# Optimization experiments

Hardware: AMD Instinct MI355X
Metric: run time of the kernel (lower is better)

Reference implementation:

```python
import jax, jax.numpy as jnp
import numpy as np
from jax import lax

# Model dims (match init_kwargs / Mamba2 defaults)
B = 8; C_IN = 512; C_OUT = 512; H = 32; W = 32; L = H * W
D_STATE = 64; D_CONV = 4; EXPAND = 2; HEADDIM = 64
D_INNER = EXPAND * C_IN            # 1024
NHEADS = D_INNER // HEADDIM        # 16
D_XBC = D_INNER + 2 * D_STATE      # 1152 (ngroups=1)
D_IN_PROJ = 2 * D_INNER + 2 * D_STATE + NHEADS
EPS = 1e-5


def setup_inputs() -> dict:
    key = jax.random.key(0)
    ks = jax.random.split(key, 16)
    x = jax.random.normal(ks[0], (B, C_IN, H, W), jnp.float32)
    ln_w = jnp.ones((C_IN,), jnp.float32)
    ln_b = jnp.zeros((C_IN,), jnp.float32)
    in_proj_w = jax.random.normal(ks[1], (D_IN_PROJ, C_IN), jnp.float32) * 0.02
    conv1d_w = jax.random.normal(ks[2], (D_XBC, D_CONV), jnp.float32) * 0.2
    conv1d_b = jax.random.normal(ks[3], (D_XBC,), jnp.float32) * 0.02
    dt0 = jax.random.uniform(ks[4], (NHEADS,), jnp.float32, 1e-3, 0.1)
    dt_bias = jnp.log(jnp.expm1(dt0))  # inverse softplus init
    A_log = jnp.log(jax.random.uniform(ks[5], (NHEADS,), jnp.float32, 1.0, 16.0))
    D = jax.random.normal(ks[6], (NHEADS,), jnp.float32)
    rms_w = jnp.ones((D_INNER,), jnp.float32)
    out_proj_w = jax.random.normal(ks[7], (C_IN, D_INNER), jnp.float32) * 0.02
    conv2d_w = jax.random.normal(ks[8], (C_OUT, C_IN), jnp.float32) * 0.04
    conv2d_b = jnp.zeros((C_OUT,), jnp.float32)
    bn_g = jnp.ones((C_OUT,), jnp.float32)
    bn_b = jnp.zeros((C_OUT,), jnp.float32)
    bn_mean = jnp.zeros((C_OUT,), jnp.float32)
    bn_var = jnp.ones((C_OUT,), jnp.float32)
    return dict(x=x, ln_w=ln_w, ln_b=ln_b, in_proj_w=in_proj_w, conv1d_w=conv1d_w,
                conv1d_b=conv1d_b, dt_bias=dt_bias, A_log=A_log, D=D, rms_w=rms_w,
                out_proj_w=out_proj_w, conv2d_w=conv2d_w, conv2d_b=conv2d_b,
                bn_g=bn_g, bn_b=bn_b, bn_mean=bn_mean, bn_var=bn_var)


def reference(x, ln_w, ln_b, in_proj_w, conv1d_w, conv1d_b, dt_bias, A_log, D,
              rms_w, out_proj_w, conv2d_w, conv2d_b, bn_g, bn_b, bn_mean, bn_var):
    Bb, C, Hh, Ww = x.shape
    Ltok = Hh * Ww
    # tokens: (B, L, C)
    t = x.reshape(Bb, C, Ltok).transpose(0, 2, 1)
    # LayerNorm over channel dim
    mu = jnp.mean(t, -1, keepdims=True)
    var = jnp.mean(jnp.square(t - mu), -1, keepdims=True)
    xn = (t - mu) * lax.rsqrt(var + EPS) * ln_w + ln_b
    # Mamba2 in_proj -> [z, xBC, dt]
    zxbcdt = jnp.einsum('blc,dc->bld', xn, in_proj_w)
    z = zxbcdt[..., :D_INNER]
    xBC = zxbcdt[..., D_INNER:D_INNER + D_XBC]
    dt = zxbcdt[..., D_INNER + D_XBC:]                       # (B, L, nheads)
    # causal depthwise conv1d + silu
    conv = lax.conv_general_dilated(xBC.transpose(0, 2, 1), conv1d_w[:, None, :],
                                    window_strides=(1,), padding=[(D_CONV - 1, 0)],
                                    feature_group_count=D_XBC)
    xBC = jax.nn.silu(conv.transpose(0, 2, 1) + conv1d_b)
    xh = xBC[..., :D_INNER].reshape(Bb, Ltok, NHEADS, HEADDIM)
    Bm = xBC[..., D_INNER:D_INNER + D_STATE]                 # (B, L, d_state)
    Cm = xBC[..., D_INNER + D_STATE:]
    dt = jax.nn.softplus(dt + dt_bias)
    A = -jnp.exp(A_log)                                      # (nheads,)
    # selective scan (SSD recurrence), state h: (B, nheads, headdim, d_state)
    def step(h, inp):
        xt, dtt, Bt, Ct = inp
        dA = jnp.exp(dtt * A)                                # (B, nheads)
        h = h * dA[..., None, None] + jnp.einsum('bh,bhp,bs->bhps', dtt, xt, Bt)
        y = jnp.einsum('bhps,bs->bhp', h, Ct)
        return h, y
    h0 = jnp.zeros((Bb, NHEADS, HEADDIM, D_STATE), x.dtype)
    xs = (xh.transpose(1, 0, 2, 3), dt.transpose(1, 0, 2),
          Bm.transpose(1, 0, 2), Cm.transpose(1, 0, 2))
    _, ys = lax.scan(step, h0, xs)
    y = ys.transpose(1, 0, 2, 3) + D[None, None, :, None] * xh
    y = y.reshape(Bb, Ltok, D_INNER)
    # gated RMSNorm
    y = y * jax.nn.silu(z)
    y = y * lax.rsqrt(jnp.mean(y * y, -1, keepdims=True) + EPS) * rms_w
    out = jnp.einsum('bld,cd->blc', y, out_proj_w)
    img = out.transpose(0, 2, 1).reshape(Bb, C, Hh, Ww)
    # 1x1 conv + BN (inference) + ReLU
    c = jnp.einsum('bchw,oc->bohw', img, conv2d_w) + conv2d_b[None, :, None, None]
    c = (c - bn_mean[None, :, None, None]) * lax.rsqrt(bn_var + EPS)[None, :, None, None]
    c = c * bn_g[None, :, None, None] + bn_b[None, :, None, None]
    return jax.nn.relu(c)
```

## Files before the change

kernel.cpp:

```cpp
#include <hip/hip_runtime.h>
#include <hip/hip_bf16.h>

#define NB 8
#define LL 1024
#define CIN 512
#define DIN 1024
#define DXBC 1152
#define DPROJ 2192
#define NPADW 2304
#define NUSE 2176
#define NHH 16
#define HDD 64
#define DST 64
#define NCHUNK 16
#define QCH 64
#define XBCS 1024
#define CTT 8
#define DTB 16

typedef unsigned short u16;
typedef unsigned int u32;
typedef __bf16 bf16x8 __attribute__((ext_vector_type(8)));
typedef float f32x4 __attribute__((ext_vector_type(4)));
typedef u16 u16x8 __attribute__((ext_vector_type(8)));

__device__ __forceinline__ float bf2f(u16 u) {
    u32 x = ((u32)u) << 16; float f; __builtin_memcpy(&f, &x, 4); return f;
}
__device__ __forceinline__ u16 f2bf(float f) {
    u32 x; __builtin_memcpy(&x, &f, 4);
    u32 r = x + 0x7fff + ((x >> 16) & 1);
    return (u16)(r >> 16);
}

__device__ __forceinline__ void gload16(const u16* g, u16* l) {
    __builtin_amdgcn_global_load_lds((__attribute__((address_space(1))) void*)(g),
                                     (__attribute__((address_space(3))) void*)(l), 16, 0, 0);
}

__device__ __forceinline__ int swz(int row, int cb) {
    return row * 64 + ((cb ^ ((row & 7) << 4)) >> 1);
}

#define PREP_WIN_BLKS 4608
#define PREP_WC2_BLKS 1024
__global__ __launch_bounds__(256) void prep_all(const float* __restrict__ ipw, u16* __restrict__ Win,
                                                const float* __restrict__ c2w, u16* __restrict__ Wc2,
                                                const float* __restrict__ cb, const float* __restrict__ g,
                                                const float* __restrict__ bb, const float* __restrict__ mean,
                                                const float* __restrict__ var,
                                                float* __restrict__ scale, float* __restrict__ shift) {
    int bid = blockIdx.x;
    if (bid < PREP_WIN_BLKS) {
        int i = bid * 256 + threadIdx.x;
        Win[i] = (i < DPROJ * CIN) ? f2bf(ipw[i]) : (u16)0;
    } else if (bid < PREP_WIN_BLKS + PREP_WC2_BLKS) {
        int i = (bid - PREP_WIN_BLKS) * 256 + threadIdx.x;
        Wc2[i] = f2bf(c2w[i]);
    } else {
        int i = (bid - PREP_WIN_BLKS - PREP_WC2_BLKS) * 256 + threadIdx.x;
        if (i < CIN) {
            float rs = rsqrtf(var[i] + 1e-5f);
            float sc = g[i] * rs;
            scale[i] = sc;
            shift[i] = (cb[i] - mean[i]) * sc + bb[i];
        }
    }
}

__global__ __launch_bounds__(256) void woutT_conv(const float* __restrict__ s,
                                                  const float* __restrict__ rw,
                                                  u16* __restrict__ dt) {
    __shared__ float tile[64][65];
    int bc = blockIdx.x & 7, bd = blockIdx.x >> 3;
    int c0 = bc * 64, d0 = bd * 64;
    int t = threadIdx.x;
    int r4 = t >> 6, cc = t & 63;
#pragma unroll
    for (int rr = 0; rr < 16; ++rr) {
        int row = r4 * 16 + rr;
        tile[row][cc] = s[(size_t)(c0 + row) * DIN + d0 + cc];
    }
    __syncthreads();
#pragma unroll
    for (int rr = 0; rr < 16; ++rr) {
        int row = r4 * 16 + rr;
        dt[(size_t)(d0 + row) * CIN + c0 + cc] = f2bf(tile[cc][row] * rw[d0 + row]);
    }
}

__global__ __launch_bounds__(256) void ln_kernel(const float* __restrict__ x,
                                                 const float* __restrict__ lw,
                                                 const float* __restrict__ lb,
                                                 u16* __restrict__ xn) {
    __shared__ u16 tile[CIN * 33];
    __shared__ float psum[8][32], psq[8][32], muA[32], rsA[32];
    int bid = blockIdx.x;
    int b = bid >> 5, hw0 = (bid & 31) * 32;
    int t = threadIdx.x;
    int hw = t & 31, cg = t >> 5;
    const float* xb = x + (size_t)b * CIN * LL + hw0 + hw;
    float s = 0.f, sq = 0.f;
    for (int r = 0; r < CIN / 8; ++r) {
        int c = r * 8 + cg;
        float v = xb[(size_t)c * LL];
        s += v; sq += v * v;
        tile[c * 33 + hw] = f2bf(v);
    }
    psum[cg][hw] = s; psq[cg][hw] = sq;
    __syncthreads();
    if (t < 32) {
        float ss = 0.f, qq = 0.f;
        for (int g = 0; g < 8; ++g) { ss += psum[g][t]; qq += psq[g][t]; }
        float mu = ss * (1.f / CIN);
        float var = qq * (1.f / CIN) - mu * mu;
        muA[t] = mu; rsA[t] = rsqrtf(var + 1e-5f);
    }
    __syncthreads();
    for (int r = 0; r < 64; ++r) {
        int idx = r * 256 + t;
        int c = idx & (CIN - 1);
        int hh = idx >> 9;
        float v = (bf2f(tile[c * 33 + hh]) - muA[hh]) * rsA[hh] * lw[c] + lb[c];
        xn[((size_t)(b * LL + hw0 + hh)) * CIN + c] = f2bf(v);
    }
}

template <int EPI>
__global__ __launch_bounds__(256) void gemm_bt(const u16* __restrict__ A, const u16* __restrict__ Bw,
                                               void* __restrict__ Cout, int M, int N, int K, int ldc,
                                               int nx,
                                               const float* __restrict__ scale,
                                               const float* __restrict__ shift,
                                               const float* __restrict__ PS) {
    __shared__ u16 As[2][128 * 64], Bs[2][64 * 64];
    __shared__ float rsl[64];
    int t = threadIdx.x;
    int lane = t & 63, wave = t >> 6;
    int nblk = gridDim.x;
    int qq = nblk >> 3, rm = nblk & 7;
    int xcd = blockIdx.x & 7, idx = blockIdx.x >> 3;
    int swzb = (xcd < rm ? xcd * (qq + 1) : rm * (qq + 1) + (xcd - rm) * qq) + idx;
    int m0 = (swzb / nx) * 128, n0 = (swzb % nx) * 64;
    int wr = wave >> 1, wc = wave & 1;
    f32x4 acc[4][2];
    for (int m = 0; m < 4; ++m)
        for (int n = 0; n < 2; ++n)
            for (int q = 0; q < 4; ++q) acc[m][n][q] = 0.f;

    if (EPI == 1) {
        if (t < 64) {
            int tok = n0 + t;
            int b = tok >> 10, rem = tok & 1023;
            int c = rem >> 6, ii = rem & 63;
            float s = 0.f;
#pragma unroll
            for (int h = 0; h < NHH; ++h)
                s += PS[(size_t)(((b << 4) + h) * 16 + c) * 64 + ii];
            rsl[t] = rsqrtf(s * (1.f / DIN) + 1e-5f);
        }
        __syncthreads();
    }

    const u16* Arow = A + (size_t)m0 * K;
    const u16* Brow = Bw + (size_t)n0 * K;
    int s4 = lane >> 4;
    int rr = lane & 15;

    auto STAGE = [&](int buf, int k0) {
#pragma unroll
        for (int j = 0; j < 4; ++j) {
            int e = j * 256 + t;
            int r = e >> 3, sr = e & 7;
            int src = (sr ^ (r & 7)) * 8;
            gload16(Arow + (size_t)r * K + k0 + src, &As[buf][e * 8]);
        }
#pragma unroll
        for (int j = 0; j < 2; ++j) {
            int e = j * 256 + t;
            int r = e >> 3, sr = e & 7;
            int src = (sr ^ (r & 7)) * 8;
            gload16(Brow + (size_t)r * K + k0 + src, &Bs[buf][e * 8]);
        }
    };

    STAGE(0, 0);
    int NK = K >> 6, cur = 0;
    for (int kt = 0; kt < NK; ++kt) {
        if (kt + 1 < NK) {
            STAGE(cur ^ 1, (kt + 1) << 6);
            asm volatile("s_waitcnt vmcnt(6)" ::: "memory");
        } else {
            asm volatile("s_waitcnt vmcnt(0)" ::: "memory");
        }
        __builtin_amdgcn_s_barrier();
        __builtin_amdgcn_sched_barrier(0);
#pragma unroll
        for (int kk = 0; kk < 2; ++kk) {
            bf16x8 af[4], bfr[2];
#pragma unroll
            for (int m = 0; m < 4; ++m) {
                int row = wr * 64 + m * 16 + rr;
                int ss = (kk * 4 + s4) ^ (row & 7);
                af[m] = *(const bf16x8*)&As[cur][row * 64 + ss * 8];
            }
#pragma unroll
            for (int n = 0; n < 2; ++n) {
                int row = wc * 32 + n * 16 + rr;
                int ss = (kk * 4 + s4) ^ (row & 7);
                bfr[n] = *(const bf16x8*)&Bs[cur][row * 64 + ss * 8];
            }
#pragma unroll
            for (int m = 0; m < 4; ++m)
#pragma unroll
                for (int n = 0; n < 2; ++n)
                    acc[m][n] = __builtin_amdgcn_mfma_f32_16x16x32_bf16(af[m], bfr[n], acc[m][n], 0, 0, 0);
        }
        __builtin_amdgcn_s_barrier();
        cur ^= 1;
    }
    int fq = lane >> 4, fr = lane & 15;
#pragma unroll
    for (int m = 0; m < 4; ++m) {
#pragma unroll
        for (int n = 0; n < 2; ++n) {
            int col = n0 + wc * 32 + n * 16 + fr;
#pragma unroll
            for (int q = 0; q < 4; ++q) {
                int row = m0 + wr * 64 + m * 16 + fq * 4 + q;
                float v = acc[m][n][q];
                if (EPI == 0) {
                    ((u16*)Cout)[(size_t)row * ldc + col] = f2bf(v);
                } else {
                    v = v * rsl[col - n0];
                    v = v * scale[row] + shift[row];
                    v = v > 0.f ? v : 0.f;
                    ((float*)Cout)[((size_t)(col >> 10)) * (CIN * LL) + (size_t)row * LL + (col & 1023)] = v;
                }
            }
        }
    }
}

__global__ __launch_bounds__(288) void convdt(const u16* __restrict__ zx,
                                              const float* __restrict__ w,
                                              const float* __restrict__ bias,
                                              u16* __restrict__ xbc,
                                              u16* __restrict__ Bc, u16* __restrict__ Cc,
                                              const u16* __restrict__ xn,
                                              const float* __restrict__ wproj,
                                              const float* __restrict__ dt_bias,
                                              const float* __restrict__ A_log,
                                              float2* __restrict__ dtda) {
    int bid = blockIdx.x;
    int t = threadIdx.x;
    if (bid < NB * (LL / CTT)) {
        int b = bid >> 7;
        int l0 = (bid & 127) * CTT;
        bool isX = t < 256;
        int ch = isX ? t * 4 : 1024 + (t - 256) * 4;

        float4 wv0 = *(const float4*)&w[(ch + 0) * 4];
        float4 wv1 = *(const float4*)&w[(ch + 1) * 4];
        float4 wv2 = *(const float4*)&w[(ch + 2) * 4];
        float4 wv3 = *(const float4*)&w[(ch + 3) * 4];
        float4 bv = *(const float4*)&bias[ch];

        ushort4 xin[CTT + 3];
        const u16* src = zx + (size_t)(b * LL + l0 - 3) * NPADW + DIN + ch;
#pragma unroll
        for (int i = 0; i < CTT + 3; ++i) {
            ushort4 v = {0, 0, 0, 0};
            if (l0 + i - 3 >= 0) v = *(const ushort4*)(src + (size_t)i * NPADW);
            xin[i] = v;
        }
#pragma unroll
        for (int i = 0; i < CTT; ++i) {
            int tok = b * LL + l0 + i;
            float a0 = bv.x + bf2f(xin[i].x) * wv0.x + bf2f(xin[i + 1].x) * wv0.y +
                       bf2f(xin[i + 2].x) * wv0.z + bf2f(xin[i + 3].x) * wv0.w;
            float a1 = bv.y + bf2f(xin[i].y) * wv1.x + bf2f(xin[i + 1].y) * wv1.y +
                       bf2f(xin[i + 2].y) * wv1.z + bf2f(xin[i + 3].y) * wv1.w;
            float a2 = bv.z + bf2f(xin[i].z) * wv2.x + bf2f(xin[i + 1].z) * wv2.y +
                       bf2f(xin[i + 2].z) * wv2.z + bf2f(xin[i + 3].z) * wv2.w;
            float a3 = bv.w + bf2f(xin[i].w) * wv3.x + bf2f(xin[i + 1].w) * wv3.y +
                       bf2f(xin[i + 2].w) * wv3.z + bf2f(xin[i + 3].w) * wv3.w;
            float s0 = a0 / (1.f + __expf(-a0));
            float s1 = a1 / (1.f + __expf(-a1));
            float s2 = a2 / (1.f + __expf(-a2));
            float s3 = a3 / (1.f + __expf(-a3));
            ushort4 o;
            o.x = f2bf(s0); o.y = f2bf(s1); o.z = f2bf(s2); o.w = f2bf(s3);
            if (isX) {
                *(ushort4*)&xbc[(size_t)tok * XBCS + ch] = o;
            } else {
                int s = ch - 1024;
                if (s < DST) *(ushort4*)&Bc[(size_t)tok * DST + s] = o;
                else         *(ushort4*)&Cc[(size_t)tok * DST + (s - DST)] = o;
            }
        }
    } else {
        if (t >= 256) return;
        int h = t >> 4, part = t & 15;
        int tok0 = (bid - NB * (LL / CTT)) * DTB;
        const float* wr = wproj + (size_t)(DIN + DXBC + h) * CIN + part * 32;
        float4 wv[8];
#pragma unroll
        for (int i = 0; i < 8; ++i) wv[i] = *(const float4*)&wr[i * 4];
        const float* wf = (const float*)wv;
        float dtb = dt_bias[h];
        float An = -__expf(A_log[h]);
#pragma unroll
        for (int tl = 0; tl < DTB; ++tl) {
            int tok = tok0 + tl;
            const u16* xr = xn + (size_t)tok * CIN + part * 32;
            u16x8 xv0 = *(const u16x8*)&xr[0];
            u16x8 xv1 = *(const u16x8*)&xr[8];
            u16x8 xv2 = *(const u16x8*)&xr[16];
            u16x8 xv3 = *(const u16x8*)&xr[24];
            float s = 0.f;
#pragma unroll
            for (int i = 0; i < 8; ++i) s += bf2f(xv0[i]) * wf[i];
#pragma unroll
            for (int i = 0; i < 8; ++i) s += bf2f(xv1[i]) * wf[8 + i];
#pragma unroll
            for (int i = 0; i < 8; ++i) s += bf2f(xv2[i]) * wf[16 + i];
#pragma unroll
            for (int i = 0; i < 8; ++i) s += bf2f(xv3[i]) * wf[24 + i];
            s += __shfl_xor(s, 1, 64);
            s += __shfl_xor(s, 2, 64);
            s += __shfl_xor(s, 4, 64);
            s += __shfl_xor(s, 8, 64);
            if (part == 0) {
                float si = s + dtb;
                float dtv = si > 15.f ? si : __logf(1.f + __expf(si));
                float2 dd; dd.x = dtv; dd.y = dtv * An;
                dtda[(size_t)tok * NHH + h] = dd;
            }
        }
    }
}

__global__ __launch_bounds__(256) void ssd_chunk(const u16* __restrict__ Bcb,
                                                 const u16* __restrict__ Ccb,
                                                 const u16* __restrict__ xbc,
                                                 const float2* __restrict__ dtda,
                                                 u16* __restrict__ yi,
                                                 u16* __restrict__ DHb,
                                                 float* __restrict__ ESA,
                                                 float* __restrict__ DC) {
    __shared__ u16 Bt[4096], Ct[4096], XT[4096], BTt[4096], Gt[4096];
    __shared__ float Sar[64], dtvA[64], wA[64];
    int tau = blockIdx.x;
    int b = tau >> 8, h = (tau >> 4) & 15, c = tau & 15;
    int t0g = b * LL + c * QCH;
    int t = threadIdx.x, lane = t & 63, wave = t >> 6;
    int row = t >> 2, q = t & 3;

    {
        const u16* bp = Bcb + (size_t)(t0g + row) * DST + q * 16;
        const u16* cp = Ccb + (size_t)(t0g + row) * DST + q * 16;
        u16x8 b0v = *(const u16x8*)bp;
        u16x8 b1v = *(const u16x8*)(bp + 8);
        *(u16x8*)&Bt[swz(row, q * 32)] = b0v;
        *(u16x8*)&Bt[swz(row, q * 32 + 16)] = b1v;
        u16x8 c0v = *(const u16x8*)cp;
        u16x8 c1v = *(const u16x8*)(cp + 8);
        *(u16x8*)&Ct[swz(row, q * 32)] = c0v;
        *(u16x8*)&Ct[swz(row, q * 32 + 16)] = c1v;
        const u16* xp = xbc + (size_t)(t0g + row) * XBCS + h * HDD + q * 16;
        u16x8 x0 = *(const u16x8*)xp;
        u16x8 x1 = *(const u16x8*)(xp + 8);
#pragma unroll
        for (int e = 0; e < 8; ++e) XT[swz(q * 16 + e, row * 2)] = x0[e];
#pragma unroll
        for (int e = 0; e < 8; ++e) XT[swz(q * 16 + 8 + e, row * 2)] = x1[e];
    }
    if (t < 64) {
        float2 dd = dtda[(size_t)(t0g + t) * NHH + h];
        float s = dd.y;
#pragma unroll
        for (int off = 1; off < 64; off <<= 1) {
            float u = __shfl_up(s, off, 64);
            if (t >= off) s += u;
        }
        float SQ = __shfl(s, 63, 64);
        Sar[t] = s; dtvA[t] = dd.x;
        wA[t] = __expf(SQ - s) * dd.x;
        ESA[(size_t)tau * 64 + t] = __expf(s);
        if (t == 0) DC[tau] = __expf(SQ);
    }
    __syncthreads();

    int R = wave >> 1, Cq = wave & 1, rr = lane & 15, sg = lane >> 4;
    f32x4 g[2][2];
#pragma unroll
    for (int mi = 0; mi < 2; ++mi)
#pragma unroll
        for (int ni = 0; ni < 2; ++ni)
#pragma unroll
            for (int r = 0; r < 4; ++r) g[mi][ni][r] = 0.f;
#pragma unroll
    for (int kt = 0; kt < 2; ++kt) {
        int cb = kt * 64 + sg * 16;
        bf16x8 a0 = *(const bf16x8*)&Ct[swz(R * 32 + rr, cb)];
        bf16x8 a1 = *(const bf16x8*)&Ct[swz(R * 32 + 16 + rr, cb)];
        bf16x8 b0 = *(const bf16x8*)&Bt[swz(Cq * 32 + rr, cb)];
        bf16x8 b1 = *(const bf16x8*)&Bt[swz(Cq * 32 + 16 + rr, cb)];
        g[0][0] = __builtin_amdgcn_mfma_f32_16x16x32_bf16(a0, b0, g[0][0], 0, 0, 0);
        g[0][1] = __builtin_amdgcn_mfma_f32_16x16x32_bf16(a0, b1, g[0][1], 0, 0, 0);
        g[1][0] = __builtin_amdgcn_mfma_f32_16x16x32_bf16(a1, b0, g[1][0], 0, 0, 0);
        g[1][1] = __builtin_amdgcn_mfma_f32_16x16x32_bf16(a1, b1, g[1][1], 0, 0, 0);
    }
#pragma unroll
    for (int mi = 0; mi < 2; ++mi)
#pragma unroll
        for (int ni = 0; ni < 2; ++ni)
#pragma unroll
            for (int r = 0; r < 4; ++r) {
                int i = R * 32 + mi * 16 + sg * 4 + r;
                int j = Cq * 32 + ni * 16 + rr;
                float v = (i >= j) ? g[mi][ni][r] * __expf(Sar[i] - Sar[j]) * dtvA[j] : 0.f;
                Gt[swz(i, j * 2)] = f2bf(v);
            }
#pragma unroll
    for (int half = 0; half < 2; ++half) {
        u16x8 bv = *(const u16x8*)&Bt[swz(row, q * 32 + half * 16)];
#pragma unroll
        for (int e = 0; e < 8; ++e)
            BTt[swz(q * 16 + half * 8 + e, row * 2)] = f2bf(bf2f(bv[e]) * wA[row]);
    }
    __syncthreads();

    f32x4 y[2][2], dh[2][2];
#pragma unroll
    for (int mi = 0; mi < 2; ++mi)
#pragma unroll
        for (int ni = 0; ni < 2; ++ni)
#pragma unroll
            for (int r = 0; r < 4; ++r) { y[mi][ni][r] = 0.f; dh[mi][ni][r] = 0.f; }
#pragma unroll
    for (int kt = 0; kt < 2; ++kt) {
        int cb = kt * 64 + sg * 16;
        bf16x8 xb0 = *(const bf16x8*)&XT[swz(Cq * 32 + rr, cb)];
        bf16x8 xb1 = *(const bf16x8*)&XT[swz(Cq * 32 + 16 + rr, cb)];
        bf16x8 ga0 = *(const bf16x8*)&Gt[swz(R * 32 + rr, cb)];
        bf16x8 ga1 = *(const bf16x8*)&Gt[swz(R * 32 + 16 + rr, cb)];
        bf16x8 ba0 = *(const bf16x8*)&BTt[swz(R * 32 + rr, cb)];
        bf16x8 ba1 = *(const bf16x8*)&BTt[swz(R * 32 + 16 + rr, cb)];
        y[0][0] = __builtin_amdgcn_mfma_f32_16x16x32_bf16(ga0, xb0, y[0][0], 0, 0, 0);
        y[0][1] = __builtin_amdgcn_mfma_f32_16x16x32_bf16(ga0, xb1, y[0][1], 0, 0, 0);
        y[1][0] = __builtin_amdgcn_mfma_f32_16x16x32_bf16(ga1, xb0, y[1][0], 0, 0, 0);
        y[1][1] = __builtin_amdgcn_mfma_f32_16x16x32_bf16(ga1, xb1, y[1][1], 0, 0, 0);
        dh[0][0] = __builtin_amdgcn_mfma_f32_16x16x32_bf16(ba0, xb0, dh[0][0], 0, 0, 0);
        dh[0][1] = __builtin_amdgcn_mfma_f32_16x16x32_bf16(ba0, xb1, dh[0][1], 0, 0, 0);
        dh[1][0] = __builtin_amdgcn_mfma_f32_16x16x32_bf16(ba1, xb0, dh[1][0], 0, 0, 0);
        dh[1][1] = __builtin_amdgcn_mfma_f32_16x16x32_bf16(ba1, xb1, dh[1][1], 0, 0, 0);
    }
#pragma unroll
    for (int mi = 0; mi < 2; ++mi)
#pragma unroll
        for (int ni = 0; ni < 2; ++ni)
#pragma unroll
            for (int r = 0; r < 4; ++r) {
                int i = R * 32 + mi * 16 + sg * 4 + r;
                int p = Cq * 32 + ni * 16 + rr;
                yi[(size_t)(t0g + i) * DIN + h * HDD + p] = f2bf(y[mi][ni][r]);
                DHb[(size_t)tau * 4096 + i * 64 + p] = f2bf(dh[mi][ni][r]);
            }
}

__global__ __launch_bounds__(256) void ssd_carry(const u16* __restrict__ DHb,
                                                 const float* __restrict__ DC,
                                                 u16* __restrict__ HPREV) {
    int bid = blockIdx.x;
    int bh = bid >> 1, ph = bid & 1;
    int t = threadIdx.x;
    int s = t >> 2, p0 = ph * 32 + (t & 3) * 8;
    size_t base = (size_t)bh * NCHUNK * 4096 + s * 64 + p0;
    float Hv[8] = {0.f, 0.f, 0.f, 0.f, 0.f, 0.f, 0.f, 0.f};
    for (int c = 0; c < NCHUNK; ++c) {
        size_t off = base + (size_t)c * 4096;
        u16x8 hp;
#pragma unroll
        for (int e = 0; e < 8; ++e) hp[e] = f2bf(Hv[e]);
        *(u16x8*)&HPREV[off] = hp;
        float d = DC[bh * NCHUNK + c];
        u16x8 dv = *(const u16x8*)&DHb[off];
#pragma unroll
        for (int e = 0; e < 8; ++e) Hv[e] = d * Hv[e] + bf2f(dv[e]);
    }
}

__global__ __launch_bounds__(256) void ssd_final(const u16* __restrict__ Ccb,
                                                 const float* __restrict__ ESA,
                                                 const u16* __restrict__ HPREV,
                                                 const u16* __restrict__ xbc,
                                                 const u16* __restrict__ zx,
                                                 const float* __restrict__ Dp,
                                                 u16* __restrict__ yi,
                                                 float* __restrict__ PS) {
    __shared__ u16 C2t[4096], HT[4096];
    __shared__ float smem_ps[2][64];
    int tau = blockIdx.x;
    int b = tau >> 8, h = (tau >> 4) & 15, c = tau & 15;
    int t0g = b * LL + c * QCH;
    int t = threadIdx.x, lane = t & 63, wave = t >> 6;
    int row = t >> 2, q = t & 3;
    {
        float esa = ESA[(size_t)tau * 64 + row];
        const u16* cp = Ccb + (size_t)(t0g + row) * DST + q * 16;
#pragma unroll
        for (int half = 0; half < 2; ++half) {
            u16x8 cv = *(const u16x8*)(cp + half * 8);
            u16x8 oc;
#pragma unroll
            for (int e = 0; e < 8; ++e) oc[e] = f2bf(bf2f(cv[e]) * esa);
            *(u16x8*)&C2t[swz(row, q * 32 + half * 16)] = oc;
            u16x8 hv = *(const u16x8*)&HPREV[(size_t)tau * 4096 + row * 64 + q * 16 + half * 8];
#pragma unroll
            for (int e = 0; e < 8; ++e) HT[swz(q * 16 + half * 8 + e, row * 2)] = hv[e];
        }
    }
    __syncthreads();
    int R = wave >> 1, Cq = wave & 1, rr = lane & 15, sg = lane >> 4;
    float Dh = Dp[h];
    f32x4 acc[2][2];
#pragma unroll
    for (int mi = 0; mi < 2; ++mi)
#pragma unroll
        for (int ni = 0; ni < 2; ++ni)
#pragma unroll
            for (int r = 0; r < 4; ++r) {
                int i = R * 32 + mi * 16 + sg * 4 + r;
                int p = Cq * 32 + ni * 16 + rr;
                acc[mi][ni][r] = bf2f(yi[(size_t)(t0g + i) * DIN + h * HDD + p]);
            }
#pragma unroll
    for (int kt = 0; kt < 2; ++kt) {
        int cb = kt * 64 + sg * 16;
        bf16x8 a0 = *(const bf16x8*)&C2t[swz(R * 32 + rr, cb)];
        bf16x8 a1 = *(const bf16x8*)&C2t[swz(R * 32 + 16 + rr, cb)];
        bf16x8 b0 = *(const bf16x8*)&HT[swz(Cq * 32 + rr, cb)];
        bf16x8 b1 = *(const bf16x8*)&HT[swz(Cq * 32 + 16 + rr, cb)];
        acc[0][0] = __builtin_amdgcn_mfma_f32_16x16x32_bf16(a0, b0, acc[0][0], 0, 0, 0);
        acc[0][1] = __builtin_amdgcn_mfma_f32_16x16x32_bf16(a0, b1, acc[0][1], 0, 0, 0);
        acc[1][0] = __builtin_amdgcn_mfma_f32_16x16x32_bf16(a1, b0, acc[1][0], 0, 0, 0);
        acc[1][1] = __builtin_amdgcn_mfma_f32_16x16x32_bf16(a1, b1, acc[1][1], 0, 0, 0);
    }
    float ps[2][4];
#pragma unroll
    for (int mi = 0; mi < 2; ++mi)
#pragma unroll
        for (int r = 0; r < 4; ++r) ps[mi][r] = 0.f;
#pragma unroll
    for (int mi = 0; mi < 2; ++mi)
#pragma unroll
        for (int ni = 0; ni < 2; ++ni)
#pragma unroll
            for (int r = 0; r < 4; ++r) {
                int i = R * 32 + mi * 16 + sg * 4 + r;
                int p = Cq * 32 + ni * 16 + rr;
                size_t tok = t0g + i;
                int col = h * HDD + p;
                float xf = bf2f(xbc[tok * XBCS + col]);
                float zf = bf2f(zx[tok * NPADW + col]);
                float yo = (acc[mi][ni][r] + Dh * xf) * (zf / (1.f + __expf(-zf)));
                yi[tok * DIN + col] = f2bf(yo);
                ps[mi][r] += yo * yo;
            }
#pragma unroll
    for (int mi = 0; mi < 2; ++mi)
#pragma unroll
        for (int r = 0; r < 4; ++r) {
            float s2 = ps[mi][r];
            s2 += __shfl_xor(s2, 1, 64);
            s2 += __shfl_xor(s2, 2, 64);
            s2 += __shfl_xor(s2, 4, 64);
            s2 += __shfl_xor(s2, 8, 64);
            if (rr == 0) smem_ps[Cq][R * 32 + mi * 16 + sg * 4 + r] = s2;
        }
    __syncthreads();
    if (t < 64) PS[(size_t)tau * 64 + t] = smem_ps[0][t] + smem_ps[1][t];
}

extern "C" void kernel_launch(void* const* d_in, const int* in_sizes, int n_in,
                              void* d_out, int out_size, void* d_ws, size_t ws_size,
                              hipStream_t stream) {
    const float* x         = (const float*)d_in[0];
    const float* ln_w      = (const float*)d_in[1];
    const float* ln_b      = (const float*)d_in[2];
    const float* in_proj_w = (const float*)d_in[3];
    const float* conv1d_w  = (const float*)d_in[4];
    const float* conv1d_b  = (const float*)d_in[5];
    const float* dt_bias   = (const float*)d_in[6];
    const float* A_log     = (const float*)d_in[7];
    const float* Dp        = (const float*)d_in[8];
    const float* rms_w     = (const float*)d_in[9];
    const float* out_proj_w= (const float*)d_in[10];
    const float* conv2d_w  = (const float*)d_in[11];
    const float* conv2d_b  = (const float*)d_in[12];
    const float* bn_g      = (const float*)d_in[13];
    const float* bn_b      = (const float*)d_in[14];
    const float* bn_mean   = (const float*)d_in[15];
    const float* bn_var    = (const float*)d_in[16];

    const int TOK = NB * LL;
    const int NTAU = NB * NHH * NCHUNK;
    char* ws = (char*)d_ws;
    size_t off = 0;
    auto alloc = [&](size_t bytes) {
        void* p = ws + off;
        off += (bytes + 255) & ~(size_t)255;
        return p;
    };
    u16*   Win   = (u16*)alloc((size_t)NPADW * CIN * 2);
    u16*   WoutT = (u16*)alloc((size_t)DIN * CIN * 2);
    u16*   Wc2   = (u16*)alloc((size_t)CIN * CIN * 2);
    u16*   WCMB  = (u16*)alloc((size_t)CIN * DIN * 2);
    u16*   XN    = (u16*)alloc((size_t)TOK * CIN * 2);
    u16*   ZX    = (u16*)alloc((size_t)TOK * NPADW * 2);
    u16*   XBC   = (u16*)alloc((size_t)TOK * XBCS * 2);
    u16*   Bcb   = (u16*)alloc((size_t)TOK * DST * 2);
    u16*   Ccb   = (u16*)alloc((size_t)TOK * DST * 2);
    float2* DTDA = (float2*)alloc((size_t)TOK * NHH * 8);
    u16*   YI    = (u16*)alloc((size_t)TOK * DIN * 2);
    u16*   DHb   = (u16*)alloc((size_t)NTAU * 4096 * 2);
    u16*   HPREV = (u16*)alloc((size_t)NTAU * 4096 * 2);
    float* ESA   = (float*)alloc((size_t)NTAU * 64 * 4);
    float* PS    = (float*)alloc((size_t)NTAU * 64 * 4);
    float* DC    = (float*)alloc((size_t)NTAU * 4);
    float* BNSC  = (float*)alloc(CIN * 4);
    float* BNSH  = (float*)alloc(CIN * 4);

    prep_all<<<PREP_WIN_BLKS + PREP_WC2_BLKS + 2, 256, 0, stream>>>(
        in_proj_w, Win, conv2d_w, Wc2, conv2d_b, bn_g, bn_b, bn_mean, bn_var, BNSC, BNSH);
    woutT_conv<<<128, 256, 0, stream>>>(out_proj_w, rms_w, WoutT);
    gemm_bt<0><<<(CIN / 128) * (DIN / 64), 256, 0, stream>>>(Wc2, WoutT, WCMB, CIN, DIN, CIN, DIN,
                                                             DIN / 64, nullptr, nullptr, nullptr);

    ln_kernel<<<256, 256, 0, stream>>>(x, ln_w, ln_b, XN);

    gemm_bt<0><<<(TOK / 128) * (NUSE / 64), 256, 0, stream>>>(XN, Win, ZX, TOK, NUSE, CIN, NPADW,
                                                              NUSE / 64, nullptr, nullptr, nullptr);

    convdt<<<NB * (LL / CTT) + TOK / DTB, 288, 0, stream>>>(ZX, conv1d_w, conv1d_b, XBC, Bcb, Ccb,
                                                            XN, in_proj_w, dt_bias, A_log, DTDA);

    ssd_chunk<<<NTAU, 256, 0, stream>>>(Bcb, Ccb, XBC, DTDA, YI, DHb, ESA, DC);
    ssd_carry<<<256, 256, 0, stream>>>(DHb, DC, HPREV);
    ssd_final<<<NTAU, 256, 0, stream>>>(Ccb, ESA, HPREV, XBC, ZX, Dp, YI, PS);

    gemm_bt<1><<<(CIN / 128) * (TOK / 64), 256, 0, stream>>>(WCMB, YI, d_out, CIN, TOK, DIN, 0,
                                                             TOK / 64, BNSC, BNSH, PS);
}
```

Measured before the change: 143.5 us.

## Fuse depthwise conv and dt projection into ssd_chunk kernel

Removes the separate convdt kernel and computes the causal depthwise conv plus SiLU, and the dt projection with softplus, directly inside ssd_chunk. Each block convolves its head's x channels and writes them to XBC for later kernels, and it also recomputes the B and C channels it needs, writing Ccb only from head 0. This saves a kernel launch and the Bcb and DTDA round trips through global memory. In exchange, the B/C conv and the dt dot product are recomputed redundantly by all 16 heads.

Result: slower. 209.4 us (+46.0%).

```diff
diff --git a/kernel.cpp b/kernel.cpp
--- a/kernel.cpp
+++ b/kernel.cpp
@@ -15,8 +15,6 @@
 #define NCHUNK 16
 #define QCH 64
 #define XBCS 1024
-#define CTT 8
-#define DTB 16
 
 typedef unsigned short u16;
 typedef unsigned int u32;
@@ -242,115 +240,21 @@
     }
 }
 
-__global__ __launch_bounds__(288) void convdt(const u16* __restrict__ zx,
-                                              const float* __restrict__ w,
-                                              const float* __restrict__ bias,
-                                              u16* __restrict__ xbc,
-                                              u16* __restrict__ Bc, u16* __restrict__ Cc,
-                                              const u16* __restrict__ xn,
-                                              const float* __restrict__ wproj,
-                                              const float* __restrict__ dt_bias,
-                                              const float* __restrict__ A_log,
-                                              float2* __restrict__ dtda) {
-    int bid = blockIdx.x;
-    int t = threadIdx.x;
-    if (bid < NB * (LL / CTT)) {
-        int b = bid >> 7;
-        int l0 = (bid & 127) * CTT;
-        bool isX = t < 256;
-        int ch = isX ? t * 4 : 1024 + (t - 256) * 4;
-
-        float4 wv0 = *(const float4*)&w[(ch + 0) * 4];
-        float4 wv1 = *(const float4*)&w[(ch + 1) * 4];
-        float4 wv2 = *(const float4*)&w[(ch + 2) * 4];
-        float4 wv3 = *(const float4*)&w[(ch + 3) * 4];
-        float4 bv = *(const float4*)&bias[ch];
-
-        ushort4 xin[CTT + 3];
-        const u16* src = zx + (size_t)(b * LL + l0 - 3) * NPADW + DIN + ch;
-#pragma unroll
-        for (int i = 0; i < CTT + 3; ++i) {
-            ushort4 v = {0, 0, 0, 0};
-            if (l0 + i - 3 >= 0) v = *(const ushort4*)(src + (size_t)i * NPADW);
-            xin[i] = v;
-        }
-#pragma unroll
-        for (int i = 0; i < CTT; ++i) {
-            int tok = b * LL + l0 + i;
-            float a0 = bv.x + bf2f(xin[i].x) * wv0.x + bf2f(xin[i + 1].x) * wv0.y +
-                       bf2f(xin[i + 2].x) * wv0.z + bf2f(xin[i + 3].x) * wv0.w;
-            float a1 = bv.y + bf2f(xin[i].y) * wv1.x + bf2f(xin[i + 1].y) * wv1.y +
-                       bf2f(xin[i + 2].y) * wv1.z + bf2f(xin[i + 3].y) * wv1.w;
-            float a2 = bv.z + bf2f(xin[i].z) * wv2.x + bf2f(xin[i + 1].z) * wv2.y +
-                       bf2f(xin[i + 2].z) * wv2.z + bf2f(xin[i + 3].z) * wv2.w;
-            float a3 = bv.w + bf2f(xin[i].w) * wv3.x + bf2f(xin[i + 1].w) * wv3.y +
-                       bf2f(xin[i + 2].w) * wv3.z + bf2f(xin[i + 3].w) * wv3.w;
-            float s0 = a0 / (1.f + __expf(-a0));
-            float s1 = a1 / (1.f + __expf(-a1));
-            float s2 = a2 / (1.f + __expf(-a2));
-            float s3 = a3 / (1.f + __expf(-a3));
-            ushort4 o;
-            o.x = f2bf(s0); o.y = f2bf(s1); o.z = f2bf(s2); o.w = f2bf(s3);
-            if (isX) {
-                *(ushort4*)&xbc[(size_t)tok * XBCS + ch] = o;
-            } else {
-                int s = ch - 1024;
-                if (s < DST) *(ushort4*)&Bc[(size_t)tok * DST + s] = o;
-                else         *(ushort4*)&Cc[(size_t)tok * DST + (s - DST)] = o;
-            }
-        }
-    } else {
-        if (t >= 256) return;
-        int h = t >> 4, part = t & 15;
-        int tok0 = (bid - NB * (LL / CTT)) * DTB;
-        const float* wr = wproj + (size_t)(DIN + DXBC + h) * CIN + part * 32;
-        float4 wv[8];
-#pragma unroll
-        for (int i = 0; i < 8; ++i) wv[i] = *(const float4*)&wr[i * 4];
-        const float* wf = (const float*)wv;
-        float dtb = dt_bias[h];
-        float An = -__expf(A_log[h]);
-#pragma unroll
-        for (int tl = 0; tl < DTB; ++tl) {
-            int tok = tok0 + tl;
-            const u16* xr = xn + (size_t)tok * CIN + part * 32;
-            u16x8 xv0 = *(const u16x8*)&xr[0];
-            u16x8 xv1 = *(const u16x8*)&xr[8];
-            u16x8 xv2 = *(const u16x8*)&xr[16];
-            u16x8 xv3 = *(const u16x8*)&xr[24];
-            float s = 0.f;
-#pragma unroll
-            for (int i = 0; i < 8; ++i) s += bf2f(xv0[i]) * wf[i];
-#pragma unroll
-            for (int i = 0; i < 8; ++i) s += bf2f(xv1[i]) * wf[8 + i];
-#pragma unroll
-            for (int i = 0; i < 8; ++i) s += bf2f(xv2[i]) * wf[16 + i];
-#pragma unroll
-            for (int i = 0; i < 8; ++i) s += bf2f(xv3[i]) * wf[24 + i];
-            s += __shfl_xor(s, 1, 64);
-            s += __shfl_xor(s, 2, 64);
-            s += __shfl_xor(s, 4, 64);
-            s += __shfl_xor(s, 8, 64);
-            if (part == 0) {
-                float si = s + dtb;
-                float dtv = si > 15.f ? si : __logf(1.f + __expf(si));
-                float2 dd; dd.x = dtv; dd.y = dtv * An;
-                dtda[(size_t)tok * NHH + h] = dd;
-            }
-        }
-    }
-}
-
-__global__ __launch_bounds__(256) void ssd_chunk(const u16* __restrict__ Bcb,
-                                                 const u16* __restrict__ Ccb,
-                                                 const u16* __restrict__ xbc,
-                                                 const float2* __restrict__ dtda,
+__global__ __launch_bounds__(256) void ssd_chunk(const u16* __restrict__ zx,
+                                                 const u16* __restrict__ xn,
+                                                 const float* __restrict__ wproj,
+                                                 const float* __restrict__ conv_w,
+                                                 const float* __restrict__ conv_b,
+                                                 const float* __restrict__ dt_bias,
+                                                 const float* __restrict__ A_log,
+                                                 u16* __restrict__ xbc,
+                                                 u16* __restrict__ Ccb,
                                                  u16* __restrict__ yi,
                                                  u16* __restrict__ DHb,
                                                  float* __restrict__ ESA,
                                                  float* __restrict__ DC) {
     __shared__ u16 Bt[4096], Ct[4096], XT[4096], BTt[4096], Gt[4096];
-    __shared__ float Sar[64], dtvA[64], wA[64];
+    __shared__ float Sar[64], dtvA[64], wA[64], dts[64];
     int tau = blockIdx.x;
     int b = tau >> 8, h = (tau >> 4) & 15, c = tau & 15;
     int t0g = b * LL + c * QCH;
@@ -358,35 +262,88 @@
     int row = t >> 2, q = t & 3;
 
     {
-        const u16* bp = Bcb + (size_t)(t0g + row) * DST + q * 16;
-        const u16* cp = Ccb + (size_t)(t0g + row) * DST + q * 16;
-        u16x8 b0v = *(const u16x8*)bp;
-        u16x8 b1v = *(const u16x8*)(bp + 8);
-        *(u16x8*)&Bt[swz(row, q * 32)] = b0v;
-        *(u16x8*)&Bt[swz(row, q * 32 + 16)] = b1v;
-        u16x8 c0v = *(const u16x8*)cp;
-        u16x8 c1v = *(const u16x8*)(cp + 8);
-        *(u16x8*)&Ct[swz(row, q * 32)] = c0v;
-        *(u16x8*)&Ct[swz(row, q * 32 + 16)] = c1v;
-        const u16* xp = xbc + (size_t)(t0g + row) * XBCS + h * HDD + q * 16;
-        u16x8 x0 = *(const u16x8*)xp;
-        u16x8 x1 = *(const u16x8*)(xp + 8);
-#pragma unroll
-        for (int e = 0; e < 8; ++e) XT[swz(q * 16 + e, row * 2)] = x0[e];
-#pragma unroll
-        for (int e = 0; e < 8; ++e) XT[swz(q * 16 + 8 + e, row * 2)] = x1[e];
-    }
+        const u16* xr = xn + (size_t)(t0g + row) * CIN + q * 128;
+        const float* wr = wproj + (size_t)(DIN + DXBC + h) * CIN + q * 128;
+        float s = 0.f;
+#pragma unroll
+        for (int i0 = 0; i0 < 128; i0 += 8) {
+            u16x8 xv = *(const u16x8*)&xr[i0];
+            float4 w0 = *(const float4*)&wr[i0];
+            float4 w1 = *(const float4*)&wr[i0 + 4];
+            s += bf2f(xv[0]) * w0.x + bf2f(xv[1]) * w0.y + bf2f(xv[2]) * w0.z + bf2f(xv[3]) * w0.w;
+            s += bf2f(xv[4]) * w1.x + bf2f(xv[5]) * w1.y + bf2f(xv[6]) * w1.z + bf2f(xv[7]) * w1.w;
+        }
+        s += __shfl_xor(s, 1, 64);
+        s += __shfl_xor(s, 2, 64);
+        if (q == 0) dts[row] = s;
+    }
+
+    auto convpass = [&](int chb, int zcol) -> u16x8 {
+        float4 cw[8];
+#pragma unroll
+        for (int e = 0; e < 8; ++e) cw[e] = *(const float4*)&conv_w[(chb + e) * 4];
+        float4 bv0 = *(const float4*)&conv_b[chb];
+        float4 bv1 = *(const float4*)&conv_b[chb + 4];
+        float a[8] = {bv0.x, bv0.y, bv0.z, bv0.w, bv1.x, bv1.y, bv1.z, bv1.w};
+        int lrow = c * QCH + row;
+#pragma unroll
+        for (int j = 0; j < 4; ++j) {
+            int l = lrow - 3 + j;
+            u16x8 v = {0, 0, 0, 0, 0, 0, 0, 0};
+            if (l >= 0) v = *(const u16x8*)&zx[(size_t)(b * LL + l) * NPADW + zcol];
+#pragma unroll
+            for (int e = 0; e < 8; ++e)
+                a[e] += bf2f(v[e]) * ((const float*)&cw[e])[j];
+        }
+        u16x8 o;
+#pragma unroll
+        for (int e = 0; e < 8; ++e) {
+            float sv = a[e] / (1.f + __expf(-a[e]));
+            o[e] = f2bf(sv);
+        }
+        return o;
+    };
+
+    {
+        int xch = h * HDD + q * 16;
+        u16x8 xa = convpass(xch, DIN + xch);
+        u16x8 xb2 = convpass(xch + 8, DIN + xch + 8);
+        *(u16x8*)&xbc[(size_t)(t0g + row) * XBCS + xch] = xa;
+        *(u16x8*)&xbc[(size_t)(t0g + row) * XBCS + xch + 8] = xb2;
+#pragma unroll
+        for (int e = 0; e < 8; ++e) XT[swz(q * 16 + e, row * 2)] = xa[e];
+#pragma unroll
+        for (int e = 0; e < 8; ++e) XT[swz(q * 16 + 8 + e, row * 2)] = xb2[e];
+        int bch = 1024 + q * 16;
+        u16x8 ba = convpass(bch, DIN + bch);
+        u16x8 bb2 = convpass(bch + 8, DIN + bch + 8);
+        *(u16x8*)&Bt[swz(row, q * 32)] = ba;
+        *(u16x8*)&Bt[swz(row, q * 32 + 16)] = bb2;
+        int cch = 1088 + q * 16;
+        u16x8 ca = convpass(cch, DIN + cch);
+        u16x8 cb2 = convpass(cch + 8, DIN + cch + 8);
+        *(u16x8*)&Ct[swz(row, q * 32)] = ca;
+        *(u16x8*)&Ct[swz(row, q * 32 + 16)] = cb2;
+        if (h == 0) {
+            *(u16x8*)&Ccb[(size_t)(t0g + row) * DST + q * 16] = ca;
+            *(u16x8*)&Ccb[(size_t)(t0g + row) * DST + q * 16 + 8] = cb2;
+        }
+    }
+    __syncthreads();
+
     if (t < 64) {
-        float2 dd = dtda[(size_t)(t0g + t) * NHH + h];
-        float s = dd.y;
+        float si = dts[t] + dt_bias[h];
+        float dtv = si > 15.f ? si : __logf(1.f + __expf(si));
+        float An = -__expf(A_log[h]);
+        float s = dtv * An;
 #pragma unroll
         for (int off = 1; off < 64; off <<= 1) {
             float u = __shfl_up(s, off, 64);
             if (t >= off) s += u;
         }
         float SQ = __shfl(s, 63, 64);
-        Sar[t] = s; dtvA[t] = dd.x;
-        wA[t] = __expf(SQ - s) * dd.x;
+        Sar[t] = s; dtvA[t] = dtv;
+        wA[t] = __expf(SQ - s) * dtv;
         ESA[(size_t)tau * 64 + t] = __expf(s);
         if (t == 0) DC[tau] = __expf(SQ);
     }
@@ -621,9 +578,7 @@
     u16*   XN    = (u16*)alloc((size_t)TOK * CIN * 2);
     u16*   ZX    = (u16*)alloc((size_t)TOK * NPADW * 2);
     u16*   XBC   = (u16*)alloc((size_t)TOK * XBCS * 2);
-    u16*   Bcb   = (u16*)alloc((size_t)TOK * DST * 2);
     u16*   Ccb   = (u16*)alloc((size_t)TOK * DST * 2);
-    float2* DTDA = (float2*)alloc((size_t)TOK * NHH * 8);
     u16*   YI    = (u16*)alloc((size_t)TOK * DIN * 2);
     u16*   DHb   = (u16*)alloc((size_t)NTAU * 4096 * 2);
     u16*   HPREV = (u16*)alloc((size_t)NTAU * 4096 * 2);
@@ -644,10 +599,8 @@
     gemm_bt<0><<<(TOK / 128) * (NUSE / 64), 256, 0, stream>>>(XN, Win, ZX, TOK, NUSE, CIN, NPADW,
                                                               NUSE / 64, nullptr, nullptr, nullptr);
 
-    convdt<<<NB * (LL / CTT) + TOK / DTB, 288, 0, stream>>>(ZX, conv1d_w, conv1d_b, XBC, Bcb, Ccb,
-                                                            XN, in_proj_w, dt_bias, A_log, DTDA);
-
-    ssd_chunk<<<NTAU, 256, 0, stream>>>(Bcb, Ccb, XBC, DTDA, YI, DHb, ESA, DC);
+    ssd_chunk<<<NTAU, 256, 0, stream>>>(ZX, XN, in_proj_w, conv1d_w, conv1d_b, dt_bias, A_log,
+                                        XBC, Ccb, YI, DHb, ESA, DC);
     ssd_carry<<<256, 256, 0, stream>>>(DHb, DC, HPREV);
     ssd_final<<<NTAU, 256, 0, stream>>>(Ccb, ESA, HPREV, XBC, ZX, Dp, YI, PS);
 
```
